# Optimization experiments

Hardware: AMD Instinct MI355X
Metric: run time of the kernel (lower is better)

Reference implementation:

```python
import jax, jax.numpy as jnp
import numpy as np

B, T, D, H = 16, 64, 256, 1536  # batch, num_seq (trg_len), input_dim, hid_dim


def setup_inputs() -> dict:
    key = jax.random.key(0)
    ks = jax.random.split(key, 6)
    def w(k, shape, fan):
        return jax.random.normal(k, shape, jnp.float32) / np.sqrt(fan).astype(np.float32)
    return {
        "batch": jax.random.normal(ks[0], (B, T, D), jnp.float32),
        # PyTorch LSTM params, gate order (i, f, g, o), layer 0 and layer 1
        "W_ih0": w(ks[1], (4 * H, D), H),
        "W_hh0": w(ks[2], (4 * H, H), H),
        "b_ih0": jnp.zeros((4 * H,), jnp.float32),
        "b_hh0": jnp.zeros((4 * H,), jnp.float32),
        "W_ih1": w(ks[3], (4 * H, H), H),
        "W_hh1": w(ks[4], (4 * H, H), H),
        "b_ih1": jnp.zeros((4 * H,), jnp.float32),
        "b_hh1": jnp.zeros((4 * H,), jnp.float32),
    }


def _lstm_cell(pre, c):
    # pre: [4H] pre-activation gates in PyTorch order i, f, g, o
    i, f, g, o = jnp.split(pre, 4, axis=-1)
    c_new = jax.nn.sigmoid(f) * c + jax.nn.sigmoid(i) * jnp.tanh(g)
    h_new = jax.nn.sigmoid(o) * jnp.tanh(c_new)
    return h_new, c_new


def reference(batch, W_ih0, W_hh0, b_ih0, b_hh0, W_ih1, W_hh1, b_ih1, b_hh1):
    hdim = W_hh0.shape[1]
    dt = batch.dtype
    # The original loop runs the unbatched 2-layer LSTM over batch[:, ei, :]
    # (length-B sequence) for ei = 1..T-1, carrying state => one scan over a
    # flattened sequence of length (T-1)*B, ordered ei-major, b-minor.
    seq = batch[:, 1:, :].transpose(1, 0, 2).reshape(-1, batch.shape[2])  # [(T-1)*B, D]
    # Precompute layer-0 input projection as one GEMM (dropout=0.3 is between
    # layers in train mode only; reference is eval mode, so no dropout).
    x_pre0 = seq @ W_ih0.T + (b_ih0 + b_hh0)  # [(T-1)*B, 4H]
    b1 = b_ih1 + b_hh1

    def step(carry, xp0):
        h, c = carry  # each [2, H] (num_layers, hid_dim), unbatched
        h0, c0 = _lstm_cell(xp0 + h[0] @ W_hh0.T, c[0])
        h1, c1 = _lstm_cell(h0 @ W_ih1.T + h[1] @ W_hh1.T + b1, c[1])
        return (jnp.stack([h0, h1]), jnp.stack([c0, c1])), None

    init = (jnp.zeros((2, hdim), dt), jnp.zeros((2, hdim), dt))
    (h_final, c_final), _ = jax.lax.scan(step, init, x_pre0)
    return h_final, c_final  # each [2, H], matching (encoder_hidden, encoder_cell)
```

## Files before the change

### kernel.cpp

```cpp
#include <hip/hip_runtime.h>
#include <cstdint>

#define HDIM   1536
#define DIN    256
#define NSTEP  1008
#define NWG    256
#define TPB    384
#define UPW    6
#define NREP   8

#define REP_W     6144
#define H1_OFF    3072
#define WS_FLAG_W (NREP*REP_W)

typedef uint32_t u32x2 __attribute__((ext_vector_type(2)));

__device__ __forceinline__ float bflo(uint32_t p){ union{uint32_t u; float f;} v; v.u = p << 16; return v.f; }
__device__ __forceinline__ float bfhi(uint32_t p){ union{uint32_t u; float f;} v; v.u = p & 0xffff0000u; return v.f; }
__device__ __forceinline__ float bf2f(uint16_t b){ union{uint32_t u; float f;} v; v.u = ((uint32_t)b) << 16; return v.f; }
__device__ __forceinline__ uint16_t f2bf(float f){
    union{float f; uint32_t u;} v; v.f = f;
    uint32_t r = v.u + 0x7fffu + ((v.u >> 16) & 1u);
    return (uint16_t)(r >> 16);
}
__device__ __forceinline__ uint32_t packbf(float lo, float hi){
    return (uint32_t)f2bf(lo) | ((uint32_t)f2bf(hi) << 16);
}
__device__ __forceinline__ float tanh_fast(float x){
    return 1.f - 2.f/(__expf(2.f*x) + 1.f);
}

#if __has_builtin(__builtin_amdgcn_fdot2_f32_bf16)
typedef __bf16 bf16x2 __attribute__((ext_vector_type(2)));
__device__ __forceinline__ float dot2bf(uint32_t a, uint32_t b, float c){
    return __builtin_amdgcn_fdot2_f32_bf16(__builtin_bit_cast(bf16x2, a),
                                           __builtin_bit_cast(bf16x2, b), c, false);
}
#else
__device__ __forceinline__ float dot2bf(uint32_t a, uint32_t b, float c){
    c = fmaf(bflo(a), bflo(b), c);
    c = fmaf(bfhi(a), bfhi(b), c);
    return c;
}
#endif

__device__ __forceinline__ float wave_sum(float x){
    #pragma unroll
    for (int o = 1; o < 64; o <<= 1) x += __shfl_xor(x, o, 64);
    return x;
}

template<int SLOW>
__device__ __forceinline__ void poll12(const char* a, uint32_t want, uint32_t pr[12]){
    u32x2 q0,q1,q2,q3,q4,q5,q6,q7,q8,q9,qa,qb;
    const uint32_t want2 = want | (want << 16);
    int t = 0;
    for (;;){
        asm volatile(
            "global_load_dwordx2 %0,  %12, off offset:-2816 sc0 sc1\n\t"
            "global_load_dwordx2 %1,  %12, off offset:-2304 sc0 sc1\n\t"
            "global_load_dwordx2 %2,  %12, off offset:-1792 sc0 sc1\n\t"
            "global_load_dwordx2 %3,  %12, off offset:-1280 sc0 sc1\n\t"
            "global_load_dwordx2 %4,  %12, off offset:-768 sc0 sc1\n\t"
            "global_load_dwordx2 %5,  %12, off offset:-256 sc0 sc1\n\t"
            "global_load_dwordx2 %6,  %12, off offset:256 sc0 sc1\n\t"
            "global_load_dwordx2 %7,  %12, off offset:768 sc0 sc1\n\t"
            "global_load_dwordx2 %8,  %12, off offset:1280 sc0 sc1\n\t"
            "global_load_dwordx2 %9,  %12, off offset:1792 sc0 sc1\n\t"
            "global_load_dwordx2 %10, %12, off offset:2304 sc0 sc1\n\t"
            "global_load_dwordx2 %11, %12, off offset:2816 sc0 sc1\n\t"
            "s_waitcnt vmcnt(0)"
            : "=v"(q0),"=v"(q1),"=v"(q2),"=v"(q3),"=v"(q4),"=v"(q5),
              "=v"(q6),"=v"(q7),"=v"(q8),"=v"(q9),"=v"(qa),"=v"(qb)
            : "v"(a) : "memory");
        uint32_t d;
        d  = __builtin_amdgcn_perm(q0.y, q0.x, 0x07060302u) ^ want2;
        d |= __builtin_amdgcn_perm(q1.y, q1.x, 0x07060302u) ^ want2;
        d |= __builtin_amdgcn_perm(q2.y, q2.x, 0x07060302u) ^ want2;
        d |= __builtin_amdgcn_perm(q3.y, q3.x, 0x07060302u) ^ want2;
        d |= __builtin_amdgcn_perm(q4.y, q4.x, 0x07060302u) ^ want2;
        d |= __builtin_amdgcn_perm(q5.y, q5.x, 0x07060302u) ^ want2;
        d |= __builtin_amdgcn_perm(q6.y, q6.x, 0x07060302u) ^ want2;
        d |= __builtin_amdgcn_perm(q7.y, q7.x, 0x07060302u) ^ want2;
        d |= __builtin_amdgcn_perm(q8.y, q8.x, 0x07060302u) ^ want2;
        d |= __builtin_amdgcn_perm(q9.y, q9.x, 0x07060302u) ^ want2;
        d |= __builtin_amdgcn_perm(qa.y, qa.x, 0x07060302u) ^ want2;
        d |= __builtin_amdgcn_perm(qb.y, qb.x, 0x07060302u) ^ want2;
        if (__all(d == 0u)) break;
        if (SLOW){
            if (t == 0) __builtin_amdgcn_s_sleep(8);
            else        __builtin_amdgcn_s_sleep(2);
        } else {
            __builtin_amdgcn_s_sleep(2);
        }
        ++t;
    }
    pr[0]  = __builtin_amdgcn_perm(q0.y, q0.x, 0x05040100u);
    pr[1]  = __builtin_amdgcn_perm(q1.y, q1.x, 0x05040100u);
    pr[2]  = __builtin_amdgcn_perm(q2.y, q2.x, 0x05040100u);
    pr[3]  = __builtin_amdgcn_perm(q3.y, q3.x, 0x05040100u);
    pr[4]  = __builtin_amdgcn_perm(q4.y, q4.x, 0x05040100u);
    pr[5]  = __builtin_amdgcn_perm(q5.y, q5.x, 0x05040100u);
    pr[6]  = __builtin_amdgcn_perm(q6.y, q6.x, 0x05040100u);
    pr[7]  = __builtin_amdgcn_perm(q7.y, q7.x, 0x05040100u);
    pr[8]  = __builtin_amdgcn_perm(q8.y, q8.x, 0x05040100u);
    pr[9]  = __builtin_amdgcn_perm(q9.y, q9.x, 0x05040100u);
    pr[10] = __builtin_amdgcn_perm(qa.y, qa.x, 0x05040100u);
    pr[11] = __builtin_amdgcn_perm(qb.y, qb.x, 0x05040100u);
}

__global__ void init_ws(const uint32_t* __restrict__ w, uint32_t* __restrict__ ws){
    const int i = blockIdx.x * blockDim.x + threadIdx.x;
    if (i < NREP*REP_W){
        const int j = i % REP_W;
        ws[i] = (j >= H1_OFF + 1536) ? 0x00010000u : 0u;
    }
    if (blockIdx.x == 0 && threadIdx.x < 64){
        const int t = threadIdx.x;
        int cnt = 0;
        #pragma unroll
        for (int j = 0; j < 4; ++j){
            const uint32_t v = w[t*4 + j];
            const uint32_t e = (v >> 7) & 0xFFu;
            if (e == 0u || (e >= 0x70u && e <= 0x7Cu)) cnt++;
        }
        #pragma unroll
        for (int o = 1; o < 64; o <<= 1) cnt += __shfl_xor(cnt, o, 64);
        if (t == 0)
            ws[WS_FLAG_W] = (cnt < 128) ? 1u : 0u;
    }
}

__global__ __launch_bounds__(TPB, 1)
void lstm_seq_kernel(const void* __restrict__ batch_,
                     const void* __restrict__ Wih0_,
                     const void* __restrict__ Whh0_,
                     const void* __restrict__ bih0_,
                     const void* __restrict__ bhh0_,
                     const void* __restrict__ Wih1_,
                     const void* __restrict__ Whh1_,
                     const void* __restrict__ bih1_,
                     const void* __restrict__ bhh1_,
                     void* __restrict__ out_,
                     uint32_t* __restrict__ ws)
{
    __shared__ uint32_t lds_w[UPW*4*8*64];
    __shared__ uint32_t lds_h0[768];
    __shared__ uint32_t lds_h1[768];
    __shared__ int      lds_flag[2];

    const int g   = blockIdx.x;
    const int tid = threadIdx.x;
    const int w   = tid >> 6;
    const int l   = tid & 63;
    const int U   = g*UPW + w;

    const uint32_t fp32in = __hip_atomic_load(&ws[WS_FLAG_W],
                             __ATOMIC_RELAXED, __HIP_MEMORY_SCOPE_AGENT);

    if (tid < 2) lds_flag[tid] = -1;

    uint32_t w0[4][14];
    uint32_t w1[4][16];
    float bb0[4], bb1[4];

    if (fp32in){
        const float2* Wih0f = (const float2*)Wih0_;
        const float2* Whh0f = (const float2*)Whh0_;
        const float2* Wih1f = (const float2*)Wih1_;
        const float2* Whh1f = (const float2*)Whh1_;
        #pragma unroll
        for (int r = 0; r < 4; ++r){
            const int grow = r*HDIM + U;
            float2 t;
            t = Wih0f[grow*(DIN/2) + l];      w0[r][0] = packbf(t.x, t.y);
            t = Wih0f[grow*(DIN/2) + 64 + l]; w0[r][1] = packbf(t.x, t.y);
            #pragma unroll
            for (int c = 0; c < 12; ++c){
                t = Whh0f[grow*(HDIM/2) + c*64 + l]; w0[r][c+2] = packbf(t.x, t.y);
            }
            #pragma unroll
            for (int c = 0; c < 8; ++c){
                t = Wih1f[grow*(HDIM/2) + c*64 + l];
                lds_w[(w*4 + r)*512 + c*64 + l] = packbf(t.x, t.y);
            }
            #pragma unroll
            for (int c = 8; c < 12; ++c){
                t = Wih1f[grow*(HDIM/2) + c*64 + l]; w1[r][c-8] = packbf(t.x, t.y);
            }
            #pragma unroll
            for (int c = 0; c < 12; ++c){
                t = Whh1f[grow*(HDIM/2) + c*64 + l]; w1[r][c+4] = packbf(t.x, t.y);
            }
            bb0[r] = ((const float*)bih0_)[grow] + ((const float*)bhh0_)[grow];
            bb1[r] = ((const float*)bih1_)[grow] + ((const float*)bhh1_)[grow];
        }
    } else {
        const uint32_t* Wih0p = (const uint32_t*)Wih0_;
        const uint32_t* Whh0p = (const uint32_t*)Whh0_;
        const uint32_t* Wih1p = (const uint32_t*)Wih1_;
        const uint32_t* Whh1p = (const uint32_t*)Whh1_;
        #pragma unroll
        for (int r = 0; r < 4; ++r){
            const int grow = r*HDIM + U;
            w0[r][0] = Wih0p[grow*(DIN/2) + l];
            w0[r][1] = Wih0p[grow*(DIN/2) + 64 + l];
            #pragma unroll
            for (int c = 0; c < 12; ++c) w0[r][c+2] = Whh0p[grow*(HDIM/2) + c*64 + l];
            #pragma unroll
            for (int c = 0; c < 8; ++c)
                lds_w[(w*4 + r)*512 + c*64 + l] = Wih1p[grow*(HDIM/2) + c*64 + l];
            #pragma unroll
            for (int c = 8; c < 12; ++c) w1[r][c-8] = Wih1p[grow*(HDIM/2) + c*64 + l];
            #pragma unroll
            for (int c = 0; c < 12; ++c) w1[r][c+4] = Whh1p[grow*(HDIM/2) + c*64 + l];
            bb0[r] = bf2f(((const uint16_t*)bih0_)[grow]) + bf2f(((const uint16_t*)bhh0_)[grow]);
            bb1[r] = bf2f(((const uint16_t*)bih1_)[grow]) + bf2f(((const uint16_t*)bhh1_)[grow]);
        }
    }
    __syncthreads();

    float c0 = 0.f, c1 = 0.f, h0f = 0.f, h1f = 0.f;
    uint32_t* wsrep = ws + (g & (NREP-1))*REP_W;

    for (int n = 0; n <= NSTEP; ++n){
        uint32_t xp0 = 0, xp1 = 0;
        if (n < NSTEP){
            const int xbase = ((n & 15)*64 + (n >> 4) + 1) * DIN;
            if (fp32in){
                const float2* bp = (const float2*)((const float*)batch_ + xbase);
                const float2 t0 = bp[l];
                const float2 t1 = bp[64 + l];
                xp0 = packbf(t0.x, t0.y); xp1 = packbf(t1.x, t1.y);
            } else {
                const uint32_t* bp = (const uint32_t*)batch_ + (xbase >> 1);
                xp0 = bp[l]; xp1 = bp[64 + l];
            }
        }

        uint32_t h0p[12];
        uint32_t h1p[12];

        if (w == 1 && n >= 1){
            const char* a = (const char*)(wsrep + H1_OFF + (n & 1)*1536) + 8*l + 2816;
            poll12<0>(a, (uint32_t)n, h1p);
            #pragma unroll
            for (int k = 0; k < 12; ++k) lds_h1[k*64 + l] = h1p[k];
            __hip_atomic_store(&lds_flag[1], n, __ATOMIC_RELEASE, __HIP_MEMORY_SCOPE_WORKGROUP);
        }

        if (w == 0){
            const char* a = (const char*)(wsrep + ((n+1) & 1)*1536) + 8*l + 2816;
            poll12<1>(a, (uint32_t)n, h0p);
            #pragma unroll
            for (int k = 0; k < 12; ++k) lds_h0[k*64 + l] = h0p[k];
            __hip_atomic_store(&lds_flag[0], n, __ATOMIC_RELEASE, __HIP_MEMORY_SCOPE_WORKGROUP);
        } else {
            while (__hip_atomic_load(&lds_flag[0], __ATOMIC_ACQUIRE, __HIP_MEMORY_SCOPE_WORKGROUP) < n)
                __builtin_amdgcn_s_sleep(1);
            #pragma unroll
            for (int k = 0; k < 12; ++k) h0p[k] = lds_h0[k*64 + l];
        }

        if (n < NSTEP){
            __builtin_amdgcn_s_setprio(1);
            float acc[4];
            #pragma unroll
            for (int r = 0; r < 4; ++r){
                float a = dot2bf(w0[r][0], xp0, 0.f);
                a = dot2bf(w0[r][1], xp1, a);
                #pragma unroll
                for (int k = 0; k < 12; ++k) a = dot2bf(w0[r][k+2], h0p[k], a);
                acc[r] = a;
            }
            #pragma unroll
            for (int r = 0; r < 4; ++r) acc[r] = wave_sum(acc[r]);
            const float gi = acc[0] + bb0[0];
            const float gf = acc[1] + bb0[1];
            const float gg = acc[2] + bb0[2];
            const float go = acc[3] + bb0[3];
            const float si = 1.f/(1.f + __expf(-gi));
            const float sf = 1.f/(1.f + __expf(-gf));
            const float so = 1.f/(1.f + __expf(-go));
            c0  = sf*c0 + si*tanh_fast(gg);
            h0f = so*tanh_fast(c0);
            const uint32_t pk = (uint32_t)f2bf(h0f) | ((uint32_t)(n + 1) << 16);
            if (l < NREP)
                __hip_atomic_store(ws + l*REP_W + (n & 1)*1536 + U, pk,
                                   __ATOMIC_RELAXED, __HIP_MEMORY_SCOPE_AGENT);
            __builtin_amdgcn_s_setprio(0);
        }

        if (n >= 1){
            if (w != 1){
                while (__hip_atomic_load(&lds_flag[1], __ATOMIC_ACQUIRE, __HIP_MEMORY_SCOPE_WORKGROUP) < n)
                    __builtin_amdgcn_s_sleep(1);
                #pragma unroll
                for (int k = 0; k < 12; ++k) h1p[k] = lds_h1[k*64 + l];
            }
            float acc[4];
            #pragma unroll
            for (int r = 0; r < 4; ++r){
                float a = 0.f;
                #pragma unroll
                for (int c = 0; c < 8; ++c)
                    a = dot2bf(lds_w[(w*4 + r)*512 + c*64 + l], h0p[c], a);
                #pragma unroll
                for (int c = 8; c < 12; ++c) a = dot2bf(w1[r][c-8], h0p[c], a);
                #pragma unroll
                for (int k = 0; k < 12; ++k) a = dot2bf(w1[r][k+4], h1p[k], a);
                acc[r] = a;
            }
            #pragma unroll
            for (int r = 0; r < 4; ++r) acc[r] = wave_sum(acc[r]);
            const float gi = acc[0] + bb1[0];
            const float gf = acc[1] + bb1[1];
            const float gg = acc[2] + bb1[2];
            const float go = acc[3] + bb1[3];
            const float si = 1.f/(1.f + __expf(-gi));
            const float sf = 1.f/(1.f + __expf(-gf));
            const float so = 1.f/(1.f + __expf(-go));
            c1  = sf*c1 + si*tanh_fast(gg);
            h1f = so*tanh_fast(c1);
            if (n < NSTEP){
                const uint32_t pk = (uint32_t)f2bf(h1f) | ((uint32_t)(n + 1) << 16);
                if (l < NREP)
                    __hip_atomic_store(ws + l*REP_W + H1_OFF + ((n+1) & 1)*1536 + U, pk,
                                       __ATOMIC_RELAXED, __HIP_MEMORY_SCOPE_AGENT);
            }
        }
    }

    if (l == 0){
        if (fp32in){
            float* o = (float*)out_;
            o[U]               = h0f;
            o[HDIM + U]        = h1f;
            o[3072 + U]        = c0;
            o[3072 + HDIM + U] = c1;
        } else {
            uint16_t* o = (uint16_t*)out_;
            o[U]               = f2bf(h0f);
            o[HDIM + U]        = f2bf(h1f);
            o[3072 + U]        = f2bf(c0);
            o[3072 + HDIM + U] = f2bf(c1);
        }
    }
}

extern "C" void kernel_launch(void* const* d_in, const int* in_sizes, int n_in,
                              void* d_out, int out_size, void* d_ws, size_t ws_size,
                              hipStream_t stream)
{
    (void)in_sizes; (void)n_in; (void)out_size; (void)ws_size;
    const void* batch = d_in[0];
    const void* Wih0  = d_in[1];
    const void* Whh0  = d_in[2];
    const void* bih0  = d_in[3];
    const void* bhh0  = d_in[4];
    const void* Wih1  = d_in[5];
    const void* Whh1  = d_in[6];
    const void* bih1  = d_in[7];
    const void* bhh1  = d_in[8];
    void* out = d_out;
    uint32_t* ws = (uint32_t*)d_ws;

    hipLaunchKernelGGL(init_ws, dim3((NREP*REP_W + 255)/256), dim3(256), 0, stream,
                       (const uint32_t*)Whh0, ws);

    void* args[] = { &batch, &Wih0, &Whh0, &bih0, &bhh0,
                     &Wih1, &Whh1, &bih1, &bhh1, &out, &ws };
    hipLaunchCooperativeKernel((const void*)lstm_seq_kernel,
                               dim3(NWG), dim3(TPB), args, 0, stream);
}
```

Measured before the change: 3.452 ms.

## Pack per-workgroup hidden states into tagged 64-bit packets and pace polling

Each workgroup now gathers its six hidden-unit outputs in LDS and one lane publishes them as two tagged 64-bit packets per replica, instead of each wave storing its own tagged 32-bit word. Consumers poll these contiguous packets with four dwordx4 loads per lane rather than twelve strided dwordx2 loads. A cycle-counter pacing scheme sleeps until shortly before the next packet is expected, which is meant to cut redundant polling traffic. The exchange layout and the LDS order of h vectors change to match. The added LDS atomic counter serialises publishing, and the pacing heuristic may wake too late and add latency.

```diff
diff --git a/kernel.cpp b/kernel.cpp
--- a/kernel.cpp
+++ b/kernel.cpp
@@ -9,11 +9,12 @@
 #define UPW    6
 #define NREP   8
 
-#define REP_W     6144
-#define H1_OFF    3072
-#define WS_FLAG_W (NREP*REP_W)
-
-typedef uint32_t u32x2 __attribute__((ext_vector_type(2)));
+#define PKT_BASE_U32(layer, par, rep)  (((((layer)*2+(par))*NREP) + (rep)) << 10)
+#define WS_FLAG_W 32768
+#define PACE_MARGIN 1400
+#define PACE_LEAK   24
+
+typedef uint32_t u32x4v __attribute__((ext_vector_type(4)));
 
 __device__ __forceinline__ float bflo(uint32_t p){ union{uint32_t u; float f;} v; v.u = p << 16; return v.f; }
 __device__ __forceinline__ float bfhi(uint32_t p){ union{uint32_t u; float f;} v; v.u = p & 0xffff0000u; return v.f; }
@@ -50,70 +51,70 @@
     return x;
 }
 
-template<int SLOW>
-__device__ __forceinline__ void poll12(const char* a, uint32_t want, uint32_t pr[12]){
-    u32x2 q0,q1,q2,q3,q4,q5,q6,q7,q8,q9,qa,qb;
+__device__ __forceinline__ void poll_gather(const uint32_t* base_u32, uint32_t want,
+                                            int l, uint32_t pr[12],
+                                            uint64_t& tprev, uint64_t& pmin, int n)
+{
+    const char* a = (const char*)base_u32 + 64*l;
+
+    if (n >= 3 && pmin > 2500 && pmin < (1ull << 40)){
+        const uint64_t tgt = tprev + pmin - PACE_MARGIN;
+        uint64_t now = __builtin_readcyclecounter();
+        while ((int64_t)(tgt - now) > 0){
+            if (tgt - now > 4096) __builtin_amdgcn_s_sleep(16);
+            else                  __builtin_amdgcn_s_sleep(2);
+            now = __builtin_readcyclecounter();
+        }
+    }
+
     const uint32_t want2 = want | (want << 16);
-    int t = 0;
+    u32x4v q0, q1, q2, q3;
     for (;;){
         asm volatile(
-            "global_load_dwordx2 %0,  %12, off offset:-2816 sc0 sc1\n\t"
-            "global_load_dwordx2 %1,  %12, off offset:-2304 sc0 sc1\n\t"
-            "global_load_dwordx2 %2,  %12, off offset:-1792 sc0 sc1\n\t"
-            "global_load_dwordx2 %3,  %12, off offset:-1280 sc0 sc1\n\t"
-            "global_load_dwordx2 %4,  %12, off offset:-768 sc0 sc1\n\t"
-            "global_load_dwordx2 %5,  %12, off offset:-256 sc0 sc1\n\t"
-            "global_load_dwordx2 %6,  %12, off offset:256 sc0 sc1\n\t"
-            "global_load_dwordx2 %7,  %12, off offset:768 sc0 sc1\n\t"
-            "global_load_dwordx2 %8,  %12, off offset:1280 sc0 sc1\n\t"
-            "global_load_dwordx2 %9,  %12, off offset:1792 sc0 sc1\n\t"
-            "global_load_dwordx2 %10, %12, off offset:2304 sc0 sc1\n\t"
-            "global_load_dwordx2 %11, %12, off offset:2816 sc0 sc1\n\t"
+            "global_load_dwordx4 %0, %4, off sc0 sc1\n\t"
+            "global_load_dwordx4 %1, %4, off offset:16 sc0 sc1\n\t"
+            "global_load_dwordx4 %2, %4, off offset:32 sc0 sc1\n\t"
+            "global_load_dwordx4 %3, %4, off offset:48 sc0 sc1\n\t"
             "s_waitcnt vmcnt(0)"
-            : "=v"(q0),"=v"(q1),"=v"(q2),"=v"(q3),"=v"(q4),"=v"(q5),
-              "=v"(q6),"=v"(q7),"=v"(q8),"=v"(q9),"=v"(qa),"=v"(qb)
+            : "=v"(q0), "=v"(q1), "=v"(q2), "=v"(q3)
             : "v"(a) : "memory");
         uint32_t d;
-        d  = __builtin_amdgcn_perm(q0.y, q0.x, 0x07060302u) ^ want2;
-        d |= __builtin_amdgcn_perm(q1.y, q1.x, 0x07060302u) ^ want2;
-        d |= __builtin_amdgcn_perm(q2.y, q2.x, 0x07060302u) ^ want2;
-        d |= __builtin_amdgcn_perm(q3.y, q3.x, 0x07060302u) ^ want2;
-        d |= __builtin_amdgcn_perm(q4.y, q4.x, 0x07060302u) ^ want2;
-        d |= __builtin_amdgcn_perm(q5.y, q5.x, 0x07060302u) ^ want2;
-        d |= __builtin_amdgcn_perm(q6.y, q6.x, 0x07060302u) ^ want2;
-        d |= __builtin_amdgcn_perm(q7.y, q7.x, 0x07060302u) ^ want2;
-        d |= __builtin_amdgcn_perm(q8.y, q8.x, 0x07060302u) ^ want2;
-        d |= __builtin_amdgcn_perm(q9.y, q9.x, 0x07060302u) ^ want2;
-        d |= __builtin_amdgcn_perm(qa.y, qa.x, 0x07060302u) ^ want2;
-        d |= __builtin_amdgcn_perm(qb.y, qb.x, 0x07060302u) ^ want2;
+        d  = __builtin_amdgcn_perm(q0.w, q0.y, 0x07060302u) ^ want2;
+        d |= __builtin_amdgcn_perm(q1.w, q1.y, 0x07060302u) ^ want2;
+        d |= __builtin_amdgcn_perm(q2.w, q2.y, 0x07060302u) ^ want2;
+        d |= __builtin_amdgcn_perm(q3.w, q3.y, 0x07060302u) ^ want2;
         if (__all(d == 0u)) break;
-        if (SLOW){
-            if (t == 0) __builtin_amdgcn_s_sleep(8);
-            else        __builtin_amdgcn_s_sleep(2);
-        } else {
-            __builtin_amdgcn_s_sleep(2);
-        }
-        ++t;
-    }
-    pr[0]  = __builtin_amdgcn_perm(q0.y, q0.x, 0x05040100u);
-    pr[1]  = __builtin_amdgcn_perm(q1.y, q1.x, 0x05040100u);
-    pr[2]  = __builtin_amdgcn_perm(q2.y, q2.x, 0x05040100u);
-    pr[3]  = __builtin_amdgcn_perm(q3.y, q3.x, 0x05040100u);
-    pr[4]  = __builtin_amdgcn_perm(q4.y, q4.x, 0x05040100u);
-    pr[5]  = __builtin_amdgcn_perm(q5.y, q5.x, 0x05040100u);
-    pr[6]  = __builtin_amdgcn_perm(q6.y, q6.x, 0x05040100u);
-    pr[7]  = __builtin_amdgcn_perm(q7.y, q7.x, 0x05040100u);
-    pr[8]  = __builtin_amdgcn_perm(q8.y, q8.x, 0x05040100u);
-    pr[9]  = __builtin_amdgcn_perm(q9.y, q9.x, 0x05040100u);
-    pr[10] = __builtin_amdgcn_perm(qa.y, qa.x, 0x05040100u);
-    pr[11] = __builtin_amdgcn_perm(qb.y, qb.x, 0x05040100u);
+        __builtin_amdgcn_s_sleep(1);
+    }
+    const uint64_t tdisc = __builtin_readcyclecounter();
+    if (n >= 1){
+        const uint64_t iv = tdisc - tprev;
+        if (iv < pmin) pmin = iv;
+        else if (pmin < (1ull << 40)) pmin += PACE_LEAK;
+    }
+    tprev = tdisc;
+
+    pr[0]  = q0.x;
+    pr[1]  = __builtin_amdgcn_perm(q0.z, q0.y, 0x05040100u);
+    pr[2]  = __builtin_amdgcn_perm(q0.w, q0.z, 0x05040302u);
+    pr[3]  = q1.x;
+    pr[4]  = __builtin_amdgcn_perm(q1.z, q1.y, 0x05040100u);
+    pr[5]  = __builtin_amdgcn_perm(q1.w, q1.z, 0x05040302u);
+    pr[6]  = q2.x;
+    pr[7]  = __builtin_amdgcn_perm(q2.z, q2.y, 0x05040100u);
+    pr[8]  = __builtin_amdgcn_perm(q2.w, q2.z, 0x05040302u);
+    pr[9]  = q3.x;
+    pr[10] = __builtin_amdgcn_perm(q3.z, q3.y, 0x05040100u);
+    pr[11] = __builtin_amdgcn_perm(q3.w, q3.z, 0x05040302u);
 }
 
 __global__ void init_ws(const uint32_t* __restrict__ w, uint32_t* __restrict__ ws){
     const int i = blockIdx.x * blockDim.x + threadIdx.x;
-    if (i < NREP*REP_W){
-        const int j = i % REP_W;
-        ws[i] = (j >= H1_OFF + 1536) ? 0x00010000u : 0u;
+    if (i < 4*NREP*1024){
+        const int region = i >> 13;
+        uint32_t v = 0u;
+        if (region == 3) v = (i & 1) ? 0x00010000u : 0u;
+        ws[i] = v;
     }
     if (blockIdx.x == 0 && threadIdx.x < 64){
         const int t = threadIdx.x;
@@ -147,6 +148,8 @@
     __shared__ uint32_t lds_w[UPW*4*8*64];
     __shared__ uint32_t lds_h0[768];
     __shared__ uint32_t lds_h1[768];
+    __shared__ uint32_t lds_pack[2][8];
+    __shared__ uint32_t lds_cnt[2];
     __shared__ int      lds_flag[2];
 
     const int g   = blockIdx.x;
@@ -154,11 +157,12 @@
     const int w   = tid >> 6;
     const int l   = tid & 63;
     const int U   = g*UPW + w;
+    const int rep = g & (NREP-1);
 
     const uint32_t fp32in = __hip_atomic_load(&ws[WS_FLAG_W],
                              __ATOMIC_RELAXED, __HIP_MEMORY_SCOPE_AGENT);
 
-    if (tid < 2) lds_flag[tid] = -1;
+    if (tid < 2){ lds_flag[tid] = -1; lds_cnt[tid] = 0u; }
 
     uint32_t w0[4][14];
     uint32_t w1[4][16];
@@ -221,7 +225,8 @@
     __syncthreads();
 
     float c0 = 0.f, c1 = 0.f, h0f = 0.f, h1f = 0.f;
-    uint32_t* wsrep = ws + (g & (NREP-1))*REP_W;
+    uint64_t t0 = 0, p0 = 1ull << 60;
+    uint64_t t1 = 0, p1 = 1ull << 60;
 
     for (int n = 0; n <= NSTEP; ++n){
         uint32_t xp0 = 0, xp1 = 0;
@@ -229,9 +234,9 @@
             const int xbase = ((n & 15)*64 + (n >> 4) + 1) * DIN;
             if (fp32in){
                 const float2* bp = (const float2*)((const float*)batch_ + xbase);
-                const float2 t0 = bp[l];
-                const float2 t1 = bp[64 + l];
-                xp0 = packbf(t0.x, t0.y); xp1 = packbf(t1.x, t1.y);
+                const float2 q0 = bp[l];
+                const float2 q1 = bp[64 + l];
+                xp0 = packbf(q0.x, q0.y); xp1 = packbf(q1.x, q1.y);
             } else {
                 const uint32_t* bp = (const uint32_t*)batch_ + (xbase >> 1);
                 xp0 = bp[l]; xp1 = bp[64 + l];
@@ -242,19 +247,21 @@
         uint32_t h1p[12];
 
         if (w == 1 && n >= 1){
-            const char* a = (const char*)(wsrep + H1_OFF + (n & 1)*1536) + 8*l + 2816;
-            poll12<0>(a, (uint32_t)n, h1p);
-            #pragma unroll
-            for (int k = 0; k < 12; ++k) lds_h1[k*64 + l] = h1p[k];
+            uint32_t pr[12];
+            poll_gather(ws + PKT_BASE_U32(1, n & 1, rep), (uint32_t)n, l, pr, t1, p1, n);
+            #pragma unroll
+            for (int k = 0; k < 12; ++k) lds_h1[12*l + k] = pr[k];
             __hip_atomic_store(&lds_flag[1], n, __ATOMIC_RELEASE, __HIP_MEMORY_SCOPE_WORKGROUP);
         }
 
         if (w == 0){
-            const char* a = (const char*)(wsrep + ((n+1) & 1)*1536) + 8*l + 2816;
-            poll12<1>(a, (uint32_t)n, h0p);
-            #pragma unroll
-            for (int k = 0; k < 12; ++k) lds_h0[k*64 + l] = h0p[k];
+            uint32_t pr[12];
+            poll_gather(ws + PKT_BASE_U32(0, (n+1) & 1, rep), (uint32_t)n, l, pr, t0, p0, n);
+            #pragma unroll
+            for (int k = 0; k < 12; ++k) lds_h0[12*l + k] = pr[k];
             __hip_atomic_store(&lds_flag[0], n, __ATOMIC_RELEASE, __HIP_MEMORY_SCOPE_WORKGROUP);
+            #pragma unroll
+            for (int k = 0; k < 12; ++k) h0p[k] = lds_h0[k*64 + l];
         } else {
             while (__hip_atomic_load(&lds_flag[0], __ATOMIC_ACQUIRE, __HIP_MEMORY_SCOPE_WORKGROUP) < n)
                 __builtin_amdgcn_s_sleep(1);
@@ -284,20 +291,37 @@
             const float so = 1.f/(1.f + __expf(-go));
             c0  = sf*c0 + si*tanh_fast(gg);
             h0f = so*tanh_fast(c0);
-            const uint32_t pk = (uint32_t)f2bf(h0f) | ((uint32_t)(n + 1) << 16);
-            if (l < NREP)
-                __hip_atomic_store(ws + l*REP_W + (n & 1)*1536 + U, pk,
-                                   __ATOMIC_RELAXED, __HIP_MEMORY_SCOPE_AGENT);
             __builtin_amdgcn_s_setprio(0);
+            if (l == 0){
+                lds_pack[0][w] = (uint32_t)f2bf(h0f);
+                const uint32_t old = __hip_atomic_fetch_add(&lds_cnt[0], 1u,
+                                        __ATOMIC_ACQ_REL, __HIP_MEMORY_SCOPE_WORKGROUP);
+                if (old == 6u*(uint32_t)n + 5u){
+                    const uint64_t tag = (uint64_t)(uint32_t)(n + 1) << 48;
+                    const uint64_t pk0 = (uint64_t)lds_pack[0][0]
+                                       | ((uint64_t)lds_pack[0][1] << 16)
+                                       | ((uint64_t)lds_pack[0][2] << 32) | tag;
+                    const uint64_t pk1 = (uint64_t)lds_pack[0][3]
+                                       | ((uint64_t)lds_pack[0][4] << 16)
+                                       | ((uint64_t)lds_pack[0][5] << 32) | tag;
+                    #pragma unroll
+                    for (int rp = 0; rp < NREP; ++rp){
+                        uint64_t* d = (uint64_t*)ws
+                            + ((uint64_t)(PKT_BASE_U32(0, n & 1, rp)) >> 1) + 2*g;
+                        __hip_atomic_store(d,   pk0, __ATOMIC_RELAXED, __HIP_MEMORY_SCOPE_AGENT);
+                        __hip_atomic_store(d+1, pk1, __ATOMIC_RELAXED, __HIP_MEMORY_SCOPE_AGENT);
+                    }
+                }
+            }
         }
 
         if (n >= 1){
             if (w != 1){
                 while (__hip_atomic_load(&lds_flag[1], __ATOMIC_ACQUIRE, __HIP_MEMORY_SCOPE_WORKGROUP) < n)
                     __builtin_amdgcn_s_sleep(1);
-                #pragma unroll
-                for (int k = 0; k < 12; ++k) h1p[k] = lds_h1[k*64 + l];
-            }
+            }
+            #pragma unroll
+            for (int k = 0; k < 12; ++k) h1p[k] = lds_h1[k*64 + l];
             float acc[4];
             #pragma unroll
             for (int r = 0; r < 4; ++r){
@@ -322,11 +346,26 @@
             const float so = 1.f/(1.f + __expf(-go));
             c1  = sf*c1 + si*tanh_fast(gg);
             h1f = so*tanh_fast(c1);
-            if (n < NSTEP){
-                const uint32_t pk = (uint32_t)f2bf(h1f) | ((uint32_t)(n + 1) << 16);
-                if (l < NREP)
-                    __hip_atomic_store(ws + l*REP_W + H1_OFF + ((n+1) & 1)*1536 + U, pk,
-                                       __ATOMIC_RELAXED, __HIP_MEMORY_SCOPE_AGENT);
+            if (n < NSTEP && l == 0){
+                lds_pack[1][w] = (uint32_t)f2bf(h1f);
+                const uint32_t old = __hip_atomic_fetch_add(&lds_cnt[1], 1u,
+                                        __ATOMIC_ACQ_REL, __HIP_MEMORY_SCOPE_WORKGROUP);
+                if (old == 6u*(uint32_t)(n - 1) + 5u){
+                    const uint64_t tag = (uint64_t)(uint32_t)(n + 1) << 48;
+                    const uint64_t pk0 = (uint64_t)lds_pack[1][0]
+                                       | ((uint64_t)lds_pack[1][1] << 16)
+                                       | ((uint64_t)lds_pack[1][2] << 32) | tag;
+                    const uint64_t pk1 = (uint64_t)lds_pack[1][3]
+                                       | ((uint64_t)lds_pack[1][4] << 16)
+                                       | ((uint64_t)lds_pack[1][5] << 32) | tag;
+                    #pragma unroll
+                    for (int rp = 0; rp < NREP; ++rp){
+                        uint64_t* d = (uint64_t*)ws
+                            + ((uint64_t)(PKT_BASE_U32(1, (n+1) & 1, rp)) >> 1) + 2*g;
+                        __hip_atomic_store(d,   pk0, __ATOMIC_RELAXED, __HIP_MEMORY_SCOPE_AGENT);
+                        __hip_atomic_store(d+1, pk1, __ATOMIC_RELAXED, __HIP_MEMORY_SCOPE_AGENT);
+                    }
+                }
             }
         }
     }
@@ -365,7 +404,7 @@
     void* out = d_out;
     uint32_t* ws = (uint32_t*)d_ws;
 
-    hipLaunchKernelGGL(init_ws, dim3((NREP*REP_W + 255)/256), dim3(256), 0, stream,
+    hipLaunchKernelGGL(init_ws, dim3((4*NREP*1024 + 255)/256), dim3(256), 0, stream,
                        (const uint32_t*)Whh0, ws);
 
     void* args[] = { &batch, &Wih0, &Whh0, &bih0, &bhh0,
```

After: 4.121 ms. 1.19x slower.

## Restructure h-state polling with contiguous per-lane chunks and double-buffered loads

Applied to the files above, without the earlier changes.

Changes the reduction layout so each lane owns a contiguous 24-element slice of the hidden state instead of strided slices. The workspace is reorganised per layer and parity so polls use wide dwordx4 loads. The layer-0 poll keeps two load batches in flight, so a new check is issued while the previous one is examined, replacing the sleep-based retry. The x input is loaded alongside the poll, and LDS h buffers are padded to a stride of 13 to avoid bank conflicts. The goal is lower latency on the per-step cross-workgroup exchange, which is the critical path, at the cost of more memory traffic from continuous polling.

```diff
diff --git a/kernel.cpp b/kernel.cpp
--- a/kernel.cpp
+++ b/kernel.cpp
@@ -9,15 +9,16 @@
 #define UPW    6
 #define NREP   8
 
-#define REP_W     6144
-#define H1_OFF    3072
-#define WS_FLAG_W (NREP*REP_W)
-
-typedef uint32_t u32x2 __attribute__((ext_vector_type(2)));
+#define XBASE(layer, par, rep) ((((layer)*2 + (par))*NREP + (rep)) * 1536)
+#define WS_FLAG_W (4*NREP*1536)
+
+typedef uint32_t u32x4v __attribute__((ext_vector_type(4)));
+typedef uint32_t u32x2v __attribute__((ext_vector_type(2)));
 
 __device__ __forceinline__ float bflo(uint32_t p){ union{uint32_t u; float f;} v; v.u = p << 16; return v.f; }
 __device__ __forceinline__ float bfhi(uint32_t p){ union{uint32_t u; float f;} v; v.u = p & 0xffff0000u; return v.f; }
 __device__ __forceinline__ float bf2f(uint16_t b){ union{uint32_t u; float f;} v; v.u = ((uint32_t)b) << 16; return v.f; }
+__device__ __forceinline__ float fbits(uint32_t u){ union{uint32_t u; float f;} v; v.u = u; return v.f; }
 __device__ __forceinline__ uint16_t f2bf(float f){
     union{float f; uint32_t u;} v; v.f = f;
     uint32_t r = v.u + 0x7fffu + ((v.u >> 16) & 1u);
@@ -50,70 +51,30 @@
     return x;
 }
 
-template<int SLOW>
-__device__ __forceinline__ void poll12(const char* a, uint32_t want, uint32_t pr[12]){
-    u32x2 q0,q1,q2,q3,q4,q5,q6,q7,q8,q9,qa,qb;
-    const uint32_t want2 = want | (want << 16);
-    int t = 0;
-    for (;;){
-        asm volatile(
-            "global_load_dwordx2 %0,  %12, off offset:-2816 sc0 sc1\n\t"
-            "global_load_dwordx2 %1,  %12, off offset:-2304 sc0 sc1\n\t"
-            "global_load_dwordx2 %2,  %12, off offset:-1792 sc0 sc1\n\t"
-            "global_load_dwordx2 %3,  %12, off offset:-1280 sc0 sc1\n\t"
-            "global_load_dwordx2 %4,  %12, off offset:-768 sc0 sc1\n\t"
-            "global_load_dwordx2 %5,  %12, off offset:-256 sc0 sc1\n\t"
-            "global_load_dwordx2 %6,  %12, off offset:256 sc0 sc1\n\t"
-            "global_load_dwordx2 %7,  %12, off offset:768 sc0 sc1\n\t"
-            "global_load_dwordx2 %8,  %12, off offset:1280 sc0 sc1\n\t"
-            "global_load_dwordx2 %9,  %12, off offset:1792 sc0 sc1\n\t"
-            "global_load_dwordx2 %10, %12, off offset:2304 sc0 sc1\n\t"
-            "global_load_dwordx2 %11, %12, off offset:2816 sc0 sc1\n\t"
-            "s_waitcnt vmcnt(0)"
-            : "=v"(q0),"=v"(q1),"=v"(q2),"=v"(q3),"=v"(q4),"=v"(q5),
-              "=v"(q6),"=v"(q7),"=v"(q8),"=v"(q9),"=v"(qa),"=v"(qb)
-            : "v"(a) : "memory");
-        uint32_t d;
-        d  = __builtin_amdgcn_perm(q0.y, q0.x, 0x07060302u) ^ want2;
-        d |= __builtin_amdgcn_perm(q1.y, q1.x, 0x07060302u) ^ want2;
-        d |= __builtin_amdgcn_perm(q2.y, q2.x, 0x07060302u) ^ want2;
-        d |= __builtin_amdgcn_perm(q3.y, q3.x, 0x07060302u) ^ want2;
-        d |= __builtin_amdgcn_perm(q4.y, q4.x, 0x07060302u) ^ want2;
-        d |= __builtin_amdgcn_perm(q5.y, q5.x, 0x07060302u) ^ want2;
-        d |= __builtin_amdgcn_perm(q6.y, q6.x, 0x07060302u) ^ want2;
-        d |= __builtin_amdgcn_perm(q7.y, q7.x, 0x07060302u) ^ want2;
-        d |= __builtin_amdgcn_perm(q8.y, q8.x, 0x07060302u) ^ want2;
-        d |= __builtin_amdgcn_perm(q9.y, q9.x, 0x07060302u) ^ want2;
-        d |= __builtin_amdgcn_perm(qa.y, qa.x, 0x07060302u) ^ want2;
-        d |= __builtin_amdgcn_perm(qb.y, qb.x, 0x07060302u) ^ want2;
-        if (__all(d == 0u)) break;
-        if (SLOW){
-            if (t == 0) __builtin_amdgcn_s_sleep(8);
-            else        __builtin_amdgcn_s_sleep(2);
-        } else {
-            __builtin_amdgcn_s_sleep(2);
-        }
-        ++t;
-    }
-    pr[0]  = __builtin_amdgcn_perm(q0.y, q0.x, 0x05040100u);
-    pr[1]  = __builtin_amdgcn_perm(q1.y, q1.x, 0x05040100u);
-    pr[2]  = __builtin_amdgcn_perm(q2.y, q2.x, 0x05040100u);
-    pr[3]  = __builtin_amdgcn_perm(q3.y, q3.x, 0x05040100u);
-    pr[4]  = __builtin_amdgcn_perm(q4.y, q4.x, 0x05040100u);
-    pr[5]  = __builtin_amdgcn_perm(q5.y, q5.x, 0x05040100u);
-    pr[6]  = __builtin_amdgcn_perm(q6.y, q6.x, 0x05040100u);
-    pr[7]  = __builtin_amdgcn_perm(q7.y, q7.x, 0x05040100u);
-    pr[8]  = __builtin_amdgcn_perm(q8.y, q8.x, 0x05040100u);
-    pr[9]  = __builtin_amdgcn_perm(q9.y, q9.x, 0x05040100u);
-    pr[10] = __builtin_amdgcn_perm(qa.y, qa.x, 0x05040100u);
-    pr[11] = __builtin_amdgcn_perm(qb.y, qb.x, 0x05040100u);
-}
+#define ISSUE6(q0,q1,q2,q3,q4,q5,addr) \
+    asm volatile("global_load_dwordx4 %0, %6, off sc0 sc1\n\t" \
+                 "global_load_dwordx4 %1, %6, off offset:16 sc0 sc1\n\t" \
+                 "global_load_dwordx4 %2, %6, off offset:32 sc0 sc1\n\t" \
+                 "global_load_dwordx4 %3, %6, off offset:48 sc0 sc1\n\t" \
+                 "global_load_dwordx4 %4, %6, off offset:64 sc0 sc1\n\t" \
+                 "global_load_dwordx4 %5, %6, off offset:80 sc0 sc1" \
+                 : "=&v"(q0),"=&v"(q1),"=&v"(q2),"=&v"(q3),"=&v"(q4),"=&v"(q5) \
+                 : "v"(addr) : "memory")
+
+#define TAG2(q) ((__builtin_amdgcn_perm((q).y,(q).x,0x07060302u)^want2) \
+               | (__builtin_amdgcn_perm((q).w,(q).z,0x07060302u)^want2))
+
+#define PAIRS2(dst,m,q) do{ \
+    (dst)[2*(m)]   = __builtin_amdgcn_perm((q).y,(q).x,0x05040100u); \
+    (dst)[2*(m)+1] = __builtin_amdgcn_perm((q).w,(q).z,0x05040100u); }while(0)
+
+#define WAITV(N) do{ asm volatile("s_waitcnt vmcnt(" #N ")" ::: "memory"); \
+                     __builtin_amdgcn_sched_barrier(0); }while(0)
 
 __global__ void init_ws(const uint32_t* __restrict__ w, uint32_t* __restrict__ ws){
     const int i = blockIdx.x * blockDim.x + threadIdx.x;
-    if (i < NREP*REP_W){
-        const int j = i % REP_W;
-        ws[i] = (j >= H1_OFF + 1536) ? 0x00010000u : 0u;
+    if (i < 4*NREP*1536){
+        ws[i] = (i >= 3*NREP*1536) ? 0x00010000u : 0u;
     }
     if (blockIdx.x == 0 && threadIdx.x < 64){
         const int t = threadIdx.x;
@@ -145,8 +106,8 @@
                      uint32_t* __restrict__ ws)
 {
     __shared__ uint32_t lds_w[UPW*4*8*64];
-    __shared__ uint32_t lds_h0[768];
-    __shared__ uint32_t lds_h1[768];
+    __shared__ uint32_t lds_h0[13*64];
+    __shared__ uint32_t lds_h1[13*64];
     __shared__ int      lds_flag[2];
 
     const int g   = blockIdx.x;
@@ -154,6 +115,7 @@
     const int w   = tid >> 6;
     const int l   = tid & 63;
     const int U   = g*UPW + w;
+    const int rep = g & (NREP-1);
 
     const uint32_t fp32in = __hip_atomic_load(&ws[WS_FLAG_W],
                              __ATOMIC_RELAXED, __HIP_MEMORY_SCOPE_AGENT);
@@ -173,24 +135,24 @@
         for (int r = 0; r < 4; ++r){
             const int grow = r*HDIM + U;
             float2 t;
-            t = Wih0f[grow*(DIN/2) + l];      w0[r][0] = packbf(t.x, t.y);
-            t = Wih0f[grow*(DIN/2) + 64 + l]; w0[r][1] = packbf(t.x, t.y);
-            #pragma unroll
-            for (int c = 0; c < 12; ++c){
-                t = Whh0f[grow*(HDIM/2) + c*64 + l]; w0[r][c+2] = packbf(t.x, t.y);
+            t = Wih0f[grow*(DIN/2) + 2*l + 0]; w0[r][0] = packbf(t.x, t.y);
+            t = Wih0f[grow*(DIN/2) + 2*l + 1]; w0[r][1] = packbf(t.x, t.y);
+            #pragma unroll
+            for (int k = 0; k < 12; ++k){
+                t = Whh0f[grow*768 + 12*l + k]; w0[r][k+2] = packbf(t.x, t.y);
             }
             #pragma unroll
             for (int c = 0; c < 8; ++c){
-                t = Wih1f[grow*(HDIM/2) + c*64 + l];
-                lds_w[(w*4 + r)*512 + c*64 + l] = packbf(t.x, t.y);
+                t = Wih1f[grow*768 + 12*l + c];
+                lds_w[((w*4 + r)*8 + c)*64 + l] = packbf(t.x, t.y);
             }
             #pragma unroll
             for (int c = 8; c < 12; ++c){
-                t = Wih1f[grow*(HDIM/2) + c*64 + l]; w1[r][c-8] = packbf(t.x, t.y);
-            }
-            #pragma unroll
-            for (int c = 0; c < 12; ++c){
-                t = Whh1f[grow*(HDIM/2) + c*64 + l]; w1[r][c+4] = packbf(t.x, t.y);
+                t = Wih1f[grow*768 + 12*l + c]; w1[r][c-8] = packbf(t.x, t.y);
+            }
+            #pragma unroll
+            for (int k = 0; k < 12; ++k){
+                t = Whh1f[grow*768 + 12*l + k]; w1[r][k+4] = packbf(t.x, t.y);
             }
             bb0[r] = ((const float*)bih0_)[grow] + ((const float*)bhh0_)[grow];
             bb1[r] = ((const float*)bih1_)[grow] + ((const float*)bhh1_)[grow];
@@ -203,63 +165,108 @@
         #pragma unroll
         for (int r = 0; r < 4; ++r){
             const int grow = r*HDIM + U;
-            w0[r][0] = Wih0p[grow*(DIN/2) + l];
-            w0[r][1] = Wih0p[grow*(DIN/2) + 64 + l];
-            #pragma unroll
-            for (int c = 0; c < 12; ++c) w0[r][c+2] = Whh0p[grow*(HDIM/2) + c*64 + l];
+            w0[r][0] = Wih0p[grow*(DIN/2) + 2*l + 0];
+            w0[r][1] = Wih0p[grow*(DIN/2) + 2*l + 1];
+            #pragma unroll
+            for (int k = 0; k < 12; ++k) w0[r][k+2] = Whh0p[grow*768 + 12*l + k];
             #pragma unroll
             for (int c = 0; c < 8; ++c)
-                lds_w[(w*4 + r)*512 + c*64 + l] = Wih1p[grow*(HDIM/2) + c*64 + l];
-            #pragma unroll
-            for (int c = 8; c < 12; ++c) w1[r][c-8] = Wih1p[grow*(HDIM/2) + c*64 + l];
-            #pragma unroll
-            for (int c = 0; c < 12; ++c) w1[r][c+4] = Whh1p[grow*(HDIM/2) + c*64 + l];
+                lds_w[((w*4 + r)*8 + c)*64 + l] = Wih1p[grow*768 + 12*l + c];
+            #pragma unroll
+            for (int c = 8; c < 12; ++c) w1[r][c-8] = Wih1p[grow*768 + 12*l + c];
+            #pragma unroll
+            for (int k = 0; k < 12; ++k) w1[r][k+4] = Whh1p[grow*768 + 12*l + k];
             bb0[r] = bf2f(((const uint16_t*)bih0_)[grow]) + bf2f(((const uint16_t*)bhh0_)[grow]);
             bb1[r] = bf2f(((const uint16_t*)bih1_)[grow]) + bf2f(((const uint16_t*)bhh1_)[grow]);
         }
     }
     __syncthreads();
 
-    float c0 = 0.f, c1 = 0.f, h0f = 0.f, h1f = 0.f;
-    uint32_t* wsrep = ws + (g & (NREP-1))*REP_W;
+    float cc0 = 0.f, cc1 = 0.f, h0f = 0.f, h1f = 0.f;
 
     for (int n = 0; n <= NSTEP; ++n){
+        const uint32_t want  = (uint32_t)n;
+        const uint32_t want2 = want | (want << 16);
+        const int nn = (n < NSTEP) ? n : 0;
+        const int xbase = ((nn & 15)*64 + (nn >> 4) + 1) * DIN;
+
+        uint32_t h0p[12], h1p[12];
         uint32_t xp0 = 0, xp1 = 0;
-        if (n < NSTEP){
-            const int xbase = ((n & 15)*64 + (n >> 4) + 1) * DIN;
+
+        if (w == 0){
+            const uint32_t* b0 = ws + XBASE(0, (n+1) & 1, rep) + 24*l;
+            u32x4v xq4; u32x2v xq2;
+            u32x4v qa0,qa1,qa2,qa3,qa4,qa5, qb0,qb1,qb2,qb3,qb4,qb5;
+
             if (fp32in){
-                const float2* bp = (const float2*)((const float*)batch_ + xbase);
-                const float2 t0 = bp[l];
-                const float2 t1 = bp[64 + l];
-                xp0 = packbf(t0.x, t0.y); xp1 = packbf(t1.x, t1.y);
+                const char* xa = (const char*)batch_ + 4*(size_t)xbase + 16*l;
+                asm volatile("global_load_dwordx4 %0, %1, off" : "=&v"(xq4) : "v"(xa) : "memory");
             } else {
-                const uint32_t* bp = (const uint32_t*)batch_ + (xbase >> 1);
-                xp0 = bp[l]; xp1 = bp[64 + l];
-            }
-        }
-
-        uint32_t h0p[12];
-        uint32_t h1p[12];
-
-        if (w == 1 && n >= 1){
-            const char* a = (const char*)(wsrep + H1_OFF + (n & 1)*1536) + 8*l + 2816;
-            poll12<0>(a, (uint32_t)n, h1p);
-            #pragma unroll
-            for (int k = 0; k < 12; ++k) lds_h1[k*64 + l] = h1p[k];
-            __hip_atomic_store(&lds_flag[1], n, __ATOMIC_RELEASE, __HIP_MEMORY_SCOPE_WORKGROUP);
-        }
-
-        if (w == 0){
-            const char* a = (const char*)(wsrep + ((n+1) & 1)*1536) + 8*l + 2816;
-            poll12<1>(a, (uint32_t)n, h0p);
-            #pragma unroll
-            for (int k = 0; k < 12; ++k) lds_h0[k*64 + l] = h0p[k];
+                const char* xa = (const char*)batch_ + 2*(size_t)xbase + 8*l;
+                asm volatile("global_load_dwordx2 %0, %1, off" : "=&v"(xq2) : "v"(xa) : "memory");
+            }
+            ISSUE6(qa0,qa1,qa2,qa3,qa4,qa5, b0);
+            ISSUE6(qb0,qb1,qb2,qb3,qb4,qb5, b0);
+            for (;;){
+                WAITV(6);
+                {
+                    const uint32_t d = TAG2(qa0)|TAG2(qa1)|TAG2(qa2)|TAG2(qa3)|TAG2(qa4)|TAG2(qa5);
+                    if (__all(d == 0u)){
+                        PAIRS2(h0p,0,qa0); PAIRS2(h0p,1,qa1); PAIRS2(h0p,2,qa2);
+                        PAIRS2(h0p,3,qa3); PAIRS2(h0p,4,qa4); PAIRS2(h0p,5,qa5);
+                        break;
+                    }
+                }
+                ISSUE6(qa0,qa1,qa2,qa3,qa4,qa5, b0);
+                WAITV(6);
+                {
+                    const uint32_t d = TAG2(qb0)|TAG2(qb1)|TAG2(qb2)|TAG2(qb3)|TAG2(qb4)|TAG2(qb5);
+                    if (__all(d == 0u)){
+                        PAIRS2(h0p,0,qb0); PAIRS2(h0p,1,qb1); PAIRS2(h0p,2,qb2);
+                        PAIRS2(h0p,3,qb3); PAIRS2(h0p,4,qb4); PAIRS2(h0p,5,qb5);
+                        break;
+                    }
+                }
+                ISSUE6(qb0,qb1,qb2,qb3,qb4,qb5, b0);
+            }
+            WAITV(0);
+
+            if (fp32in){ xp0 = packbf(fbits(xq4.x), fbits(xq4.y));
+                         xp1 = packbf(fbits(xq4.z), fbits(xq4.w)); }
+            else       { xp0 = xq2.x; xp1 = xq2.y; }
+
+            #pragma unroll
+            for (int k = 0; k < 12; ++k) lds_h0[13*l + k] = h0p[k];
             __hip_atomic_store(&lds_flag[0], n, __ATOMIC_RELEASE, __HIP_MEMORY_SCOPE_WORKGROUP);
         } else {
+            if (fp32in){
+                const float4 t = ((const float4*)((const float*)batch_ + xbase))[l];
+                xp0 = packbf(t.x, t.y); xp1 = packbf(t.z, t.w);
+            } else {
+                const uint2 t = ((const uint2*)((const uint16_t*)batch_ + xbase))[l];
+                xp0 = t.x; xp1 = t.y;
+            }
+            if (w == 1){
+                const uint32_t* b1 = ws + XBASE(1, n & 1, rep) + 24*l;
+                u32x4v t0,t1,t2,t3,t4,t5;
+                WAITV(0);
+                for (;;){
+                    ISSUE6(t0,t1,t2,t3,t4,t5, b1);
+                    WAITV(0);
+                    const uint32_t d = TAG2(t0)|TAG2(t1)|TAG2(t2)|TAG2(t3)|TAG2(t4)|TAG2(t5);
+                    if (__all(d == 0u)) break;
+                    __builtin_amdgcn_s_sleep(1);
+                }
+                PAIRS2(h1p,0,t0); PAIRS2(h1p,1,t1); PAIRS2(h1p,2,t2);
+                PAIRS2(h1p,3,t3); PAIRS2(h1p,4,t4); PAIRS2(h1p,5,t5);
+                #pragma unroll
+                for (int k = 0; k < 12; ++k) lds_h1[13*l + k] = h1p[k];
+                __hip_atomic_store(&lds_flag[1], n, __ATOMIC_RELEASE, __HIP_MEMORY_SCOPE_WORKGROUP);
+            }
             while (__hip_atomic_load(&lds_flag[0], __ATOMIC_ACQUIRE, __HIP_MEMORY_SCOPE_WORKGROUP) < n)
                 __builtin_amdgcn_s_sleep(1);
             #pragma unroll
-            for (int k = 0; k < 12; ++k) h0p[k] = lds_h0[k*64 + l];
+            for (int k = 0; k < 12; ++k) h0p[k] = lds_h0[13*l + k];
         }
 
         if (n < NSTEP){
@@ -282,13 +289,13 @@
             const float si = 1.f/(1.f + __expf(-gi));
             const float sf = 1.f/(1.f + __expf(-gf));
             const float so = 1.f/(1.f + __expf(-go));
-            c0  = sf*c0 + si*tanh_fast(gg);
-            h0f = so*tanh_fast(c0);
+            cc0 = sf*cc0 + si*tanh_fast(gg);
+            h0f = so*tanh_fast(cc0);
+            __builtin_amdgcn_s_setprio(0);
             const uint32_t pk = (uint32_t)f2bf(h0f) | ((uint32_t)(n + 1) << 16);
             if (l < NREP)
-                __hip_atomic_store(ws + l*REP_W + (n & 1)*1536 + U, pk,
+                __hip_atomic_store(ws + XBASE(0, n & 1, l) + U, pk,
                                    __ATOMIC_RELAXED, __HIP_MEMORY_SCOPE_AGENT);
-            __builtin_amdgcn_s_setprio(0);
         }
 
         if (n >= 1){
@@ -296,7 +303,7 @@
                 while (__hip_atomic_load(&lds_flag[1], __ATOMIC_ACQUIRE, __HIP_MEMORY_SCOPE_WORKGROUP) < n)
                     __builtin_amdgcn_s_sleep(1);
                 #pragma unroll
-                for (int k = 0; k < 12; ++k) h1p[k] = lds_h1[k*64 + l];
+                for (int k = 0; k < 12; ++k) h1p[k] = lds_h1[13*l + k];
             }
             float acc[4];
             #pragma unroll
@@ -304,7 +311,7 @@
                 float a = 0.f;
                 #pragma unroll
                 for (int c = 0; c < 8; ++c)
-                    a = dot2bf(lds_w[(w*4 + r)*512 + c*64 + l], h0p[c], a);
+                    a = dot2bf(lds_w[((w*4 + r)*8 + c)*64 + l], h0p[c], a);
                 #pragma unroll
                 for (int c = 8; c < 12; ++c) a = dot2bf(w1[r][c-8], h0p[c], a);
                 #pragma unroll
@@ -320,12 +327,12 @@
             const float si = 1.f/(1.f + __expf(-gi));
             const float sf = 1.f/(1.f + __expf(-gf));
             const float so = 1.f/(1.f + __expf(-go));
-            c1  = sf*c1 + si*tanh_fast(gg);
-            h1f = so*tanh_fast(c1);
+            cc1 = sf*cc1 + si*tanh_fast(gg);
+            h1f = so*tanh_fast(cc1);
             if (n < NSTEP){
                 const uint32_t pk = (uint32_t)f2bf(h1f) | ((uint32_t)(n + 1) << 16);
                 if (l < NREP)
-                    __hip_atomic_store(ws + l*REP_W + H1_OFF + ((n+1) & 1)*1536 + U, pk,
+                    __hip_atomic_store(ws + XBASE(1, (n+1) & 1, l) + U, pk,
                                        __ATOMIC_RELAXED, __HIP_MEMORY_SCOPE_AGENT);
             }
         }
@@ -336,14 +343,14 @@
             float* o = (float*)out_;
             o[U]               = h0f;
             o[HDIM + U]        = h1f;
-            o[3072 + U]        = c0;
-            o[3072 + HDIM + U] = c1;
+            o[3072 + U]        = cc0;
+            o[3072 + HDIM + U] = cc1;
         } else {
             uint16_t* o = (uint16_t*)out_;
             o[U]               = f2bf(h0f);
             o[HDIM + U]        = f2bf(h1f);
-            o[3072 + U]        = f2bf(c0);
-            o[3072 + HDIM + U] = f2bf(c1);
+            o[3072 + U]        = f2bf(cc0);
+            o[3072 + HDIM + U] = f2bf(cc1);
         }
     }
 }
@@ -365,7 +372,7 @@
     void* out = d_out;
     uint32_t* ws = (uint32_t*)d_ws;
 
-    hipLaunchKernelGGL(init_ws, dim3((NREP*REP_W + 255)/256), dim3(256), 0, stream,
+    hipLaunchKernelGGL(init_ws, dim3((4*NREP*1536 + 255)/256), dim3(256), 0, stream,
                        (const uint32_t*)Whh0, ws);
 
     void* args[] = { &batch, &Wih0, &Whh0, &bih0, &bhh0,
```

Measured after the change: 4.503 ms. 1.3x slower.
